# Optimization experiments

Measured on AMD Instinct MI355X. Metric: run time of the kernel, lower is better.

The kernel has to match this reference:

```python
import jax, jax.numpy as jnp
import numpy as np
from jax import lax

K = 5          # kernel_size
P = K // 2     # padding
DN = ('NCHW', 'OIHW', 'NCHW')


def _dwconv(z, wt, bt):
    # depthwise conv: z [b,c,h,w], wt [c,1,K,K], bt [c]
    c = z.shape[1]
    y = lax.conv_general_dilated(z, wt, (1, 1), [(P, P), (P, P)],
                                 feature_group_count=c, dimension_numbers=DN)
    return y + bt[None, :, None, None]


def setup_inputs() -> dict:
    key = jax.random.key(0)
    ks = jax.random.split(key, 8)
    b, c, h, w = 8, 64, 256, 256
    return {
        'x': jax.random.normal(ks[0], (b, c, h, w), jnp.float32),
        'w1': jax.random.normal(ks[1], (3, c, 1, K, K), jnp.float32) * 0.1,
        'b1': jax.random.normal(ks[2], (3, c), jnp.float32) * 0.1,
        'w2': jax.random.normal(ks[3], (3, c, 1, K, K), jnp.float32) * 0.1,
        'b2': jax.random.normal(ks[4], (3, c), jnp.float32) * 0.1,
        'wk': jax.random.normal(ks[5], (K * K * c, c), jnp.float32) * 0.1,
        'bk': jax.random.normal(ks[6], (K * K * c,), jnp.float32) * 0.1,
        'bias': jnp.zeros((c,), jnp.float32),
    }


def reference(x, w1, b1, w2, b2, wk, bk, bias):
    b, c, h, w = x.shape
    # avgpool 2x2 stride 2
    t = x.reshape(b, c, h // 2, 2, w // 2, 2).mean(axis=(3, 5))
    # Block1: 3 depthwise convs
    for i in range(3):
        t = _dwconv(t, w1[i], b1[i])
    # maxpool 2x2 stride 2
    hh, ww = t.shape[2], t.shape[3]
    t = t.reshape(b, c, hh // 2, 2, ww // 2, 2).max(axis=(3, 5))
    # Block2: 3 depthwise convs
    for i in range(3):
        t = _dwconv(t, w2[i], b2[i])
    # adaptive avg pool to 1x1 -> [b, c]
    g = t.mean(axis=(2, 3))
    # tokernel 1x1 conv -> per-sample depthwise kernels [b*c, 1, K, K]
    kern = (jnp.einsum('bc,oc->bo', g, wk) + bk).reshape(b * c, 1, K, K)
    # per-sample dynamic depthwise conv (groups = b*c)
    y = lax.conv_general_dilated(x.reshape(1, b * c, h, w), kern, (1, 1),
                                 [(P, P), (P, P)], feature_group_count=b * c,
                                 dimension_numbers=DN)
    return y.reshape(b, c, h, w) + bias[None, :, None, None]
```

## Files before the change

kernel.cpp:

```cpp
#include <hip/hip_runtime.h>

#define BB 8
#define CC 64
#define HH 256
#define WW 256
#define H1 128
#define W1 128
#define KK 5

template<int SS>
__device__ __forceinline__ void conv4x4(const float* __restrict__ src,
                                        const float* __restrict__ wr,
                                        float bv, float a[4][4])
{
#pragma unroll
    for (int i = 0; i < 4; i++)
#pragma unroll
        for (int j = 0; j < 4; j++) a[i][j] = bv;
#pragma unroll
    for (int ir = 0; ir < 8; ir++) {
        const float* s = src + ir * SS;
        float4 L = *(const float4*)s;
        float4 R = *(const float4*)(s + 4);
        float e[8] = {L.x, L.y, L.z, L.w, R.x, R.y, R.z, R.w};
#pragma unroll
        for (int i = 0; i < 4; i++) {
            const int ky = ir - i;
            if (ky >= 0 && ky < 5) {
#pragma unroll
                for (int kx = 0; kx < 5; kx++) {
                    const float wv = wr[ky * 5 + kx];
#pragma unroll
                    for (int j = 0; j < 4; j++) a[i][j] += e[j + kx] * wv;
                }
            }
        }
    }
}

template<int SS>
__device__ __forceinline__ void conv1x4(const float* __restrict__ src,
                                        const float* __restrict__ wr,
                                        float bv, float a[4])
{
#pragma unroll
    for (int j = 0; j < 4; j++) a[j] = bv;
#pragma unroll
    for (int ir = 0; ir < 5; ir++) {
        const float* s = src + ir * SS;
        float4 L = *(const float4*)s;
        float4 R = *(const float4*)(s + 4);
        float e[8] = {L.x, L.y, L.z, L.w, R.x, R.y, R.z, R.w};
#pragma unroll
        for (int kx = 0; kx < 5; kx++) {
            const float wv = wr[ir * 5 + kx];
#pragma unroll
            for (int j = 0; j < 4; j++) a[j] += e[j + kx] * wv;
        }
    }
}

__global__ __launch_bounds__(1024, 8) void k_a(
    const float* __restrict__ x, const float* __restrict__ w1,
    const float* __restrict__ b1, const float* __restrict__ w2,
    const float* __restrict__ b2, float* __restrict__ g)
{
    const int plane = blockIdx.x;
    const int c = plane & 63;
    const int tid = threadIdx.x;

    __shared__ __align__(16) float sA[132 * 132];
    __shared__ float red[16];

    const float* xp = x + (size_t)plane * HH * WW;

#pragma unroll
    for (int k = 0; k < 9; k++) {
        int i = tid + k * 1024;
        if (i < 132 * 66) {
            int r = i / 66, c2 = i % 66;
            float2 v = make_float2(0.f, 0.f);
            if (r >= 2 && r < 130 && c2 >= 1 && c2 <= 64) {
                int pr = r - 2;
                int xc = 4 * c2 - 4;
                float4 a0 = *(const float4*)(xp + (size_t)(2 * pr) * WW + xc);
                float4 a1 = *(const float4*)(xp + (size_t)(2 * pr + 1) * WW + xc);
                v.x = 0.25f * (a0.x + a0.y + a1.x + a1.y);
                v.y = 0.25f * (a0.z + a0.w + a1.z + a1.w);
            }
            *(float2*)&sA[r * 132 + 2 * c2] = v;
        }
    }
    __syncthreads();

    {
        const int tr = (tid >> 5) * 4, tc = (tid & 31) * 4;
#pragma unroll
        for (int cv = 0; cv < 3; cv++) {
            float wr[25];
#pragma unroll
            for (int k = 0; k < 25; k++) wr[k] = w1[cv * CC * 25 + c * 25 + k];
            const float bv = b1[cv * CC + c];
            float a[4][4];
            conv4x4<132>(&sA[tr * 132 + tc], wr, bv, a);
            __syncthreads();
#pragma unroll
            for (int i = 0; i < 4; i++) {
                float2* d = (float2*)&sA[(tr + i + 2) * 132 + tc + 2];
                d[0] = make_float2(a[i][0], a[i][1]);
                d[1] = make_float2(a[i][2], a[i][3]);
            }
            __syncthreads();
        }
    }

    float* pB = sA;
    float* pC = sA + 5440;
    float m[4];
    const int mr = (tid * 4) >> 6;
    const int mc0 = (tid * 4) & 63;
#pragma unroll
    for (int k = 0; k < 4; k++) {
        const float* p = &sA[(size_t)(2 * mr + 2) * 132 + 2 * (mc0 + k) + 2];
        m[k] = fmaxf(fmaxf(p[0], p[1]), fmaxf(p[132], p[133]));
    }
    __syncthreads();
#pragma unroll
    for (int k = 0; k < 4; k++)
        pB[(mr + 2) * 76 + mc0 + k + 2] = m[k];
    for (int i = tid; i < 1072 + 5168; i += 1024) {
        if (i < 1072) {
            int idx;
            if (i < 304) {
                int rr = i / 76;
                int rowz = (rr < 2) ? rr : 64 + rr;
                idx = rowz * 76 + (i % 76);
            } else {
                int j = i - 304;
                int row = 2 + j / 12, k2 = j % 12;
                int col = (k2 < 2) ? k2 : 64 + k2;
                idx = row * 76 + col;
            }
            pB[idx] = 0.f;
        } else {
            pC[i - 1072] = 0.f;
        }
    }
    __syncthreads();

    const int r = tid >> 4, c0 = (tid & 15) * 4;
    {
        float wr[25];
#pragma unroll
        for (int k = 0; k < 25; k++) wr[k] = w2[0 * CC * 25 + c * 25 + k];
        float a[4];
        conv1x4<76>(&pB[r * 76 + c0], wr, b2[0 * CC + c], a);
        float2* d = (float2*)&pC[(r + 2) * 76 + c0 + 2];
        d[0] = make_float2(a[0], a[1]);
        d[1] = make_float2(a[2], a[3]);
    }
    __syncthreads();
    {
        float wr[25];
#pragma unroll
        for (int k = 0; k < 25; k++) wr[k] = w2[1 * CC * 25 + c * 25 + k];
        float a[4];
        conv1x4<76>(&pC[r * 76 + c0], wr, b2[1 * CC + c], a);
        float2* d = (float2*)&pB[(r + 2) * 76 + c0 + 2];
        d[0] = make_float2(a[0], a[1]);
        d[1] = make_float2(a[2], a[3]);
    }
    __syncthreads();
    float s;
    {
        float wr[25];
#pragma unroll
        for (int k = 0; k < 25; k++) wr[k] = w2[2 * CC * 25 + c * 25 + k];
        float a[4];
        conv1x4<76>(&pB[r * 76 + c0], wr, b2[2 * CC + c], a);
        s = a[0] + a[1] + a[2] + a[3];
    }
#pragma unroll
    for (int off = 32; off > 0; off >>= 1) s += __shfl_down(s, off);
    if ((tid & 63) == 0) red[tid >> 6] = s;
    __syncthreads();
    if (tid == 0) {
        float t = 0.f;
#pragma unroll
        for (int k = 0; k < 16; k++) t += red[k];
        g[plane] = t * (1.f / 4096.f);
    }
}

__global__ __launch_bounds__(256) void k_kern(
    const float* __restrict__ g, const float* __restrict__ wk,
    const float* __restrict__ bk, float* __restrict__ kern)
{
    const int o = blockIdx.x * 256 + threadIdx.x;
    const int b = o / 1600, oo = o - b * 1600;
    float v = bk[oo];
    const float* wp = wk + (size_t)oo * 64;
    const float* gp = g + b * 64;
#pragma unroll 16
    for (int k = 0; k < 64; k++) v += gp[k] * wp[k];
    kern[o] = v;
}

__global__ __launch_bounds__(256) void k_dyn(
    const float* __restrict__ x, const float* __restrict__ kern,
    const float* __restrict__ bias, float* __restrict__ out)
{
    const int plane = blockIdx.z;
    const int tx = blockIdx.x, ty = blockIdx.y;
    const int tid = threadIdx.x;

    __shared__ __align__(16) float sx[68 * 76];

    const float* xp = x + (size_t)plane * HH * WW;
    const int R0 = ty * 64, C0 = tx * 64;

#pragma unroll
    for (int k = 0; k < 5; k++) {
        int i = tid + k * 256;
        if (i < 68 * 18) {
            int r = i / 18, q = i - r * 18;
            int gr = R0 - 2 + r;
            int gc = C0 - 4 + 4 * q;
            float4 v = make_float4(0.f, 0.f, 0.f, 0.f);
            if ((unsigned)gr < HH && (unsigned)gc < WW)
                v = *(const float4*)(xp + (size_t)gr * WW + gc);
            *(float4*)&sx[r * 76 + 4 * q] = v;
        }
    }

    float w[25];
#pragma unroll
    for (int k = 0; k < 25; k++) w[k] = kern[(size_t)plane * 25 + k];
    const float bv = bias[plane & 63];

    __syncthreads();

    const int tr = (tid >> 4) * 4;
    const int tc = (tid & 15) * 4;
    float acc[4][4];
#pragma unroll
    for (int i = 0; i < 4; i++)
#pragma unroll
        for (int j = 0; j < 4; j++) acc[i][j] = bv;

#pragma unroll
    for (int ir = 0; ir < 8; ir++) {
        const float* s = &sx[(tr + ir) * 76 + tc];
        float4 A = *(const float4*)s;
        float4 B4 = *(const float4*)(s + 4);
        float4 Cv = *(const float4*)(s + 8);
        float e[12] = {A.x, A.y, A.z, A.w, B4.x, B4.y, B4.z, B4.w,
                       Cv.x, Cv.y, Cv.z, Cv.w};
#pragma unroll
        for (int i = 0; i < 4; i++) {
            const int ky = ir - i;
            if (ky >= 0 && ky < 5) {
#pragma unroll
                for (int kx = 0; kx < 5; kx++) {
                    const float wv = w[ky * 5 + kx];
#pragma unroll
                    for (int j = 0; j < 4; j++) acc[i][j] += e[j + kx + 2] * wv;
                }
            }
        }
    }

    float* op = out + (size_t)plane * HH * WW + (size_t)(R0 + tr) * WW + C0 + tc;
#pragma unroll
    for (int i = 0; i < 4; i++)
        *(float4*)(op + (size_t)i * WW) = make_float4(acc[i][0], acc[i][1], acc[i][2], acc[i][3]);
}

extern "C" void kernel_launch(void* const* d_in, const int* in_sizes, int n_in,
                              void* d_out, int out_size, void* d_ws, size_t ws_size,
                              hipStream_t stream)
{
    const float* x    = (const float*)d_in[0];
    const float* w1   = (const float*)d_in[1];
    const float* b1   = (const float*)d_in[2];
    const float* w2   = (const float*)d_in[3];
    const float* b2   = (const float*)d_in[4];
    const float* wk   = (const float*)d_in[5];
    const float* bk   = (const float*)d_in[6];
    const float* bias = (const float*)d_in[7];
    float* out = (float*)d_out;

    float* ws   = (float*)d_ws;
    float* g    = ws;
    float* kern = ws + 512;

    k_a<<<dim3(512), 1024, 0, stream>>>(x, w1, b1, w2, b2, g);
    k_kern<<<dim3(50), 256, 0, stream>>>(g, wk, bk, kern);
    k_dyn<<<dim3(4, 4, 512), 256, 0, stream>>>(x, kern, bias, out);
}
```

Before: 116.4 us.

## Realign shared-memory tiles for float4 access and fuse maxpool into last conv

Pads the pooled plane rows to 140 floats with an 8-float left halo so that all shared-memory reads and writes in the block-1 and block-2 convs become aligned float4 accesses. The avgpool fill now produces float4 writes from two float4 global loads per row. The maxpool is fused into the third block-1 conv's register outputs, which removes a separate shared-memory pass and its barrier. Each conv now reads 12 floats per row instead of 8, and LDS use grows with the wider row stride.

After: 114.9 us. No clear change (-1.3%).

```diff
diff --git a/kernel.cpp b/kernel.cpp
--- a/kernel.cpp
+++ b/kernel.cpp
@@ -1,17 +1,15 @@
 #include <hip/hip_runtime.h>
 
-#define BB 8
 #define CC 64
 #define HH 256
 #define WW 256
-#define H1 128
-#define W1 128
-#define KK 5
+#define SROW 140
+#define BROW 76
 
 template<int SS>
-__device__ __forceinline__ void conv4x4(const float* __restrict__ src,
-                                        const float* __restrict__ wr,
-                                        float bv, float a[4][4])
+__device__ __forceinline__ void conv4x4_e12(const float* __restrict__ rb,
+                                            const float* __restrict__ w,
+                                            float bv, float a[4][4])
 {
 #pragma unroll
     for (int i = 0; i < 4; i++)
@@ -19,43 +17,46 @@
         for (int j = 0; j < 4; j++) a[i][j] = bv;
 #pragma unroll
     for (int ir = 0; ir < 8; ir++) {
-        const float* s = src + ir * SS;
-        float4 L = *(const float4*)s;
-        float4 R = *(const float4*)(s + 4);
-        float e[8] = {L.x, L.y, L.z, L.w, R.x, R.y, R.z, R.w};
+        const float* s = rb + ir * SS;
+        float4 A = *(const float4*)s;
+        float4 B = *(const float4*)(s + 4);
+        float4 C = *(const float4*)(s + 8);
+        float e[12] = {A.x, A.y, A.z, A.w, B.x, B.y, B.z, B.w,
+                       C.x, C.y, C.z, C.w};
 #pragma unroll
         for (int i = 0; i < 4; i++) {
             const int ky = ir - i;
             if (ky >= 0 && ky < 5) {
 #pragma unroll
                 for (int kx = 0; kx < 5; kx++) {
-                    const float wv = wr[ky * 5 + kx];
-#pragma unroll
-                    for (int j = 0; j < 4; j++) a[i][j] += e[j + kx] * wv;
+                    const float wv = w[ky * 5 + kx];
+#pragma unroll
+                    for (int j = 0; j < 4; j++) a[i][j] += e[j + kx + 2] * wv;
                 }
             }
         }
     }
 }
 
-template<int SS>
-__device__ __forceinline__ void conv1x4(const float* __restrict__ src,
-                                        const float* __restrict__ wr,
-                                        float bv, float a[4])
+__device__ __forceinline__ void conv1x4_e12B(const float* __restrict__ rb,
+                                             const float* __restrict__ w,
+                                             float bv, float a[4])
 {
 #pragma unroll
     for (int j = 0; j < 4; j++) a[j] = bv;
 #pragma unroll
     for (int ir = 0; ir < 5; ir++) {
-        const float* s = src + ir * SS;
-        float4 L = *(const float4*)s;
-        float4 R = *(const float4*)(s + 4);
-        float e[8] = {L.x, L.y, L.z, L.w, R.x, R.y, R.z, R.w};
+        const float* s = rb + ir * BROW;
+        float4 A = *(const float4*)s;
+        float4 B = *(const float4*)(s + 4);
+        float4 C = *(const float4*)(s + 8);
+        float e[12] = {A.x, A.y, A.z, A.w, B.x, B.y, B.z, B.w,
+                       C.x, C.y, C.z, C.w};
 #pragma unroll
         for (int kx = 0; kx < 5; kx++) {
-            const float wv = wr[ir * 5 + kx];
-#pragma unroll
-            for (int j = 0; j < 4; j++) a[j] += e[j + kx] * wv;
+            const float wv = w[ir * 5 + kx];
+#pragma unroll
+            for (int j = 0; j < 4; j++) a[j] += e[j + kx + 2] * wv;
         }
     }
 }
@@ -69,115 +70,113 @@
     const int c = plane & 63;
     const int tid = threadIdx.x;
 
-    __shared__ __align__(16) float sA[132 * 132];
+    __shared__ __align__(16) float sb[132 * SROW];
     __shared__ float red[16];
+    float* Bb = sb;
 
     const float* xp = x + (size_t)plane * HH * WW;
 
 #pragma unroll
-    for (int k = 0; k < 9; k++) {
+    for (int k = 0; k < 5; k++) {
         int i = tid + k * 1024;
-        if (i < 132 * 66) {
-            int r = i / 66, c2 = i % 66;
-            float2 v = make_float2(0.f, 0.f);
-            if (r >= 2 && r < 130 && c2 >= 1 && c2 <= 64) {
-                int pr = r - 2;
-                int xc = 4 * c2 - 4;
-                float4 a0 = *(const float4*)(xp + (size_t)(2 * pr) * WW + xc);
-                float4 a1 = *(const float4*)(xp + (size_t)(2 * pr + 1) * WW + xc);
-                v.x = 0.25f * (a0.x + a0.y + a1.x + a1.y);
-                v.y = 0.25f * (a0.z + a0.w + a1.z + a1.w);
+        if (i < 132 * 35) {
+            int r = i / 35, f = i % 35;
+            int d = 4 * f;
+            float4 v = make_float4(0.f, 0.f, 0.f, 0.f);
+            int p = r - 2;
+            if (d >= 8 && d < 136 && (unsigned)p < 128u) {
+                int xc = 2 * (d - 8);
+                const float* p0 = xp + (size_t)(2 * p) * WW + xc;
+                const float* p1 = p0 + WW;
+                float4 a0 = *(const float4*)p0;
+                float4 a1 = *(const float4*)(p0 + 4);
+                float4 b0 = *(const float4*)p1;
+                float4 b1v = *(const float4*)(p1 + 4);
+                v.x = 0.25f * (a0.x + a0.y + b0.x + b0.y);
+                v.y = 0.25f * (a0.z + a0.w + b0.z + b0.w);
+                v.z = 0.25f * (a1.x + a1.y + b1v.x + b1v.y);
+                v.w = 0.25f * (a1.z + a1.w + b1v.z + b1v.w);
             }
-            *(float2*)&sA[r * 132 + 2 * c2] = v;
-        }
-    }
-    __syncthreads();
+            *(float4*)&sb[r * SROW + d] = v;
+        }
+    }
+    __syncthreads();
+
+    const int v = tid >> 5, u = tid & 31;
+    const float* rbA = &sb[(4 * v) * SROW + 4 * u + 4];
+    float* wbA = &sb[(4 * v + 2) * SROW + 8 + 4 * u];
+
+#pragma unroll
+    for (int cv = 0; cv < 2; cv++) {
+        float w[25];
+#pragma unroll
+        for (int k = 0; k < 25; k++) w[k] = w1[cv * CC * 25 + c * 25 + k];
+        const float bv = b1[cv * CC + c];
+        float a[4][4];
+        conv4x4_e12<SROW>(rbA, w, bv, a);
+        __syncthreads();
+#pragma unroll
+        for (int i = 0; i < 4; i++)
+            *(float4*)(wbA + i * SROW) = make_float4(a[i][0], a[i][1], a[i][2], a[i][3]);
+        __syncthreads();
+    }
 
     {
-        const int tr = (tid >> 5) * 4, tc = (tid & 31) * 4;
-#pragma unroll
-        for (int cv = 0; cv < 3; cv++) {
-            float wr[25];
-#pragma unroll
-            for (int k = 0; k < 25; k++) wr[k] = w1[cv * CC * 25 + c * 25 + k];
-            const float bv = b1[cv * CC + c];
-            float a[4][4];
-            conv4x4<132>(&sA[tr * 132 + tc], wr, bv, a);
-            __syncthreads();
-#pragma unroll
-            for (int i = 0; i < 4; i++) {
-                float2* d = (float2*)&sA[(tr + i + 2) * 132 + tc + 2];
-                d[0] = make_float2(a[i][0], a[i][1]);
-                d[1] = make_float2(a[i][2], a[i][3]);
-            }
-            __syncthreads();
-        }
-    }
-
-    float* pB = sA;
-    float* pC = sA + 5440;
-    float m[4];
-    const int mr = (tid * 4) >> 6;
-    const int mc0 = (tid * 4) & 63;
-#pragma unroll
-    for (int k = 0; k < 4; k++) {
-        const float* p = &sA[(size_t)(2 * mr + 2) * 132 + 2 * (mc0 + k) + 2];
-        m[k] = fmaxf(fmaxf(p[0], p[1]), fmaxf(p[132], p[133]));
-    }
-    __syncthreads();
-#pragma unroll
-    for (int k = 0; k < 4; k++)
-        pB[(mr + 2) * 76 + mc0 + k + 2] = m[k];
-    for (int i = tid; i < 1072 + 5168; i += 1024) {
-        if (i < 1072) {
+        float w[25];
+#pragma unroll
+        for (int k = 0; k < 25; k++) w[k] = w1[2 * CC * 25 + c * 25 + k];
+        const float bv = b1[2 * CC + c];
+        float a[4][4];
+        conv4x4_e12<SROW>(rbA, w, bv, a);
+        __syncthreads();
+#pragma unroll
+        for (int ii = 0; ii < 2; ii++) {
+            float m0 = fmaxf(fmaxf(a[2 * ii][0], a[2 * ii][1]),
+                             fmaxf(a[2 * ii + 1][0], a[2 * ii + 1][1]));
+            float m1 = fmaxf(fmaxf(a[2 * ii][2], a[2 * ii][3]),
+                             fmaxf(a[2 * ii + 1][2], a[2 * ii + 1][3]));
+            *(float2*)&Bb[(2 * v + 2 + ii) * BROW + 8 + 2 * u] = make_float2(m0, m1);
+        }
+        for (int i = tid; i < 1072; i += 1024) {
             int idx;
             if (i < 304) {
-                int rr = i / 76;
+                int rr = i / BROW;
                 int rowz = (rr < 2) ? rr : 64 + rr;
-                idx = rowz * 76 + (i % 76);
+                idx = rowz * BROW + (i % BROW);
             } else {
                 int j = i - 304;
                 int row = 2 + j / 12, k2 = j % 12;
-                int col = (k2 < 2) ? k2 : 64 + k2;
-                idx = row * 76 + col;
+                int col = (k2 < 8) ? k2 : 64 + k2;
+                idx = row * BROW + col;
             }
-            pB[idx] = 0.f;
-        } else {
-            pC[i - 1072] = 0.f;
-        }
-    }
-    __syncthreads();
-
-    const int r = tid >> 4, c0 = (tid & 15) * 4;
-    {
-        float wr[25];
-#pragma unroll
-        for (int k = 0; k < 25; k++) wr[k] = w2[0 * CC * 25 + c * 25 + k];
+            Bb[idx] = 0.f;
+        }
+    }
+    __syncthreads();
+
+    const int q = tid >> 4, u2 = tid & 15;
+    const float* rbB = &Bb[q * BROW + 4 * u2 + 4];
+    float* wbB = &Bb[(q + 2) * BROW + 8 + 4 * u2];
+
+#pragma unroll
+    for (int cv = 0; cv < 2; cv++) {
+        float w[25];
+#pragma unroll
+        for (int k = 0; k < 25; k++) w[k] = w2[cv * CC * 25 + c * 25 + k];
         float a[4];
-        conv1x4<76>(&pB[r * 76 + c0], wr, b2[0 * CC + c], a);
-        float2* d = (float2*)&pC[(r + 2) * 76 + c0 + 2];
-        d[0] = make_float2(a[0], a[1]);
-        d[1] = make_float2(a[2], a[3]);
-    }
-    __syncthreads();
-    {
-        float wr[25];
-#pragma unroll
-        for (int k = 0; k < 25; k++) wr[k] = w2[1 * CC * 25 + c * 25 + k];
-        float a[4];
-        conv1x4<76>(&pC[r * 76 + c0], wr, b2[1 * CC + c], a);
-        float2* d = (float2*)&pB[(r + 2) * 76 + c0 + 2];
-        d[0] = make_float2(a[0], a[1]);
-        d[1] = make_float2(a[2], a[3]);
-    }
-    __syncthreads();
+        conv1x4_e12B(rbB, w, b2[cv * CC + c], a);
+        __syncthreads();
+        *(float4*)wbB = make_float4(a[0], a[1], a[2], a[3]);
+        __syncthreads();
+    }
+
     float s;
     {
-        float wr[25];
-#pragma unroll
-        for (int k = 0; k < 25; k++) wr[k] = w2[2 * CC * 25 + c * 25 + k];
+        float w[25];
+#pragma unroll
+        for (int k = 0; k < 25; k++) w[k] = w2[2 * CC * 25 + c * 25 + k];
         float a[4];
-        conv1x4<76>(&pB[r * 76 + c0], wr, b2[2 * CC + c], a);
+        conv1x4_e12B(rbB, w, b2[2 * CC + c], a);
         s = a[0] + a[1] + a[2] + a[3];
     }
 #pragma unroll
@@ -240,35 +239,9 @@
 
     __syncthreads();
 
-    const int tr = (tid >> 4) * 4;
-    const int tc = (tid & 15) * 4;
+    const int tr = (tid >> 4) * 4, tc = (tid & 15) * 4;
     float acc[4][4];
-#pragma unroll
-    for (int i = 0; i < 4; i++)
-#pragma unroll
-        for (int j = 0; j < 4; j++) acc[i][j] = bv;
-
-#pragma unroll
-    for (int ir = 0; ir < 8; ir++) {
-        const float* s = &sx[(tr + ir) * 76 + tc];
-        float4 A = *(const float4*)s;
-        float4 B4 = *(const float4*)(s + 4);
-        float4 Cv = *(const float4*)(s + 8);
-        float e[12] = {A.x, A.y, A.z, A.w, B4.x, B4.y, B4.z, B4.w,
-                       Cv.x, Cv.y, Cv.z, Cv.w};
-#pragma unroll
-        for (int i = 0; i < 4; i++) {
-            const int ky = ir - i;
-            if (ky >= 0 && ky < 5) {
-#pragma unroll
-                for (int kx = 0; kx < 5; kx++) {
-                    const float wv = w[ky * 5 + kx];
-#pragma unroll
-                    for (int j = 0; j < 4; j++) acc[i][j] += e[j + kx + 2] * wv;
-                }
-            }
-        }
-    }
+    conv4x4_e12<76>(&sx[tr * 76 + tc], w, bv, acc);
 
     float* op = out + (size_t)plane * HH * WW + (size_t)(R0 + tr) * WW + C0 + tc;
 #pragma unroll
```
